# Performance work log

Hardware: AMD Instinct MI355X
Metric: run time of the kernel (lower is better)

## Reference

```python
import jax, jax.numpy as jnp
import numpy as np

B, S, HID = 1, 4096, 2048
NH, NKV, D = 16, 4, 128           # num_heads, num_kv_heads, head_dim
QPG = NH // NKV                   # q heads per kv group
GROUP = (QPG + 2) * D             # fused per-group width: Q..Q K V
TOTAL = NKV * GROUP


def setup_inputs() -> dict:
    key = jax.random.key(0)
    k0, k1, k2 = jax.random.split(key, 3)
    x = jax.random.normal(k0, (B, S, HID), dtype=jnp.float32)
    weight_qkv = jax.random.normal(k1, (TOTAL, HID), dtype=jnp.float32) * 0.02
    weight_proj = jax.random.normal(k2, (HID, NH * D), dtype=jnp.float32) * 0.02
    return {"x": x, "weight_qkv": weight_qkv, "weight_proj": weight_proj}


def reference(x, weight_qkv, weight_proj):
    b, s, _ = x.shape
    # fused QKV projection, grouped layout: [b, s, NKV, (QPG+2)*D]
    qkv = jnp.einsum('bsh,ph->bsp', x, weight_qkv).reshape(b, s, NKV, GROUP)
    q = qkv[..., : QPG * D].reshape(b, s, NKV, QPG, D)      # [b,s,g,q,d]
    k = qkv[..., QPG * D:(QPG + 1) * D]                      # [b,s,g,d]
    v = qkv[..., (QPG + 1) * D:]                             # [b,s,g,d]

    scale = 1.0 / jnp.sqrt(jnp.float32(D))
    # GQA causal attention (ring attention at cp_size=1 == full causal attn)
    scores = jnp.einsum('bsgqd,btgd->bgqst', q, k) * scale   # [b,g,q,s,s]
    causal = jnp.tril(jnp.ones((s, s), dtype=bool))
    scores = jnp.where(causal, scores, jnp.finfo(scores.dtype).min)
    attn = jax.nn.softmax(scores, axis=-1)
    out = jnp.einsum('bgqst,btgd->bsgqd', attn, v)           # [b,s,g,q,d]
    out = out.reshape(b, s, NH * D)
    return jnp.einsum('bse,he->bsh', out, weight_proj)       # [b,s,HID]
```

## Files before the change

### kernel.cpp

```cpp
#include <hip/hip_runtime.h>
#include <hip/hip_bf16.h>
#include <stdint.h>

typedef __attribute__((ext_vector_type(8))) short short8;
typedef __attribute__((ext_vector_type(4))) float f32x4;

#define S_LEN   4096
#define HID_DIM 2048
#define NHEAD   16
#define NKV     4
#define DHEAD   128
#define QPG     4
#define GROUP   768
#define TOTAL   3072

__device__ __forceinline__ ushort f2bf(float f) {
    union { float f; uint32_t u; } c; c.f = f;
    uint32_t u = c.u;
    u += 0x7fff + ((u >> 16) & 1);
    return (ushort)(u >> 16);
}

__device__ __forceinline__ void gld_lds16(const void* g, void* l) {
    __builtin_amdgcn_global_load_lds(
        (const __attribute__((address_space(1))) void*)g,
        (__attribute__((address_space(3))) void*)l, 16, 0, 0);
}

__global__ __launch_bounds__(256)
void cvt_f32_bf16(const float* __restrict__ src, ushort* __restrict__ dst,
                  int n4, int mode)
{
    int i = blockIdx.x * blockDim.x + threadIdx.x;
    int stride = gridDim.x * blockDim.x;
    for (; i < n4; i += stride) {
        float sc = 1.0f;
        if (mode == 1) {
            int row = i >> 9;
            sc = ((row % GROUP) < QPG * DHEAD) ? 0.088388347648318447f : 1.0f;
        }
        float4 v = ((const float4*)src)[i];
        ushort4 o;
        o.x = f2bf(v.x * sc); o.y = f2bf(v.y * sc);
        o.z = f2bf(v.z * sc); o.w = f2bf(v.w * sc);
        ((ushort4*)dst)[i] = o;
    }
}

__global__ __launch_bounds__(256)
void zero_f4(float4* __restrict__ p, int n4)
{
    int i = blockIdx.x * blockDim.x + threadIdx.x;
    int stride = gridDim.x * blockDim.x;
    float4 z = {0.f, 0.f, 0.f, 0.f};
    for (; i < n4; i += stride) p[i] = z;
}

__device__ __forceinline__ void store_c(ushort* C, size_t idx, float v) { C[idx] = f2bf(v); }
__device__ __forceinline__ void store_c(float*  C, size_t idx, float v) { C[idx] = v; }

template <typename OutT, bool WRITE_VT>
__global__ __launch_bounds__(256, 2)
void gemm_bt(const ushort* __restrict__ A, const ushort* __restrict__ B,
             OutT* __restrict__ C, ushort* __restrict__ VT,
             int M, int N, int K)
{
    __shared__ alignas(16) ushort Asl[128 * 32];
    __shared__ alignas(16) ushort Bsl[128 * 32];

    const int tid  = threadIdx.x;
    const int wave = tid >> 6;
    const int lane = tid & 63;
    const int quad = lane >> 4;
    const int l15  = lane & 15;
    const int wr   = wave >> 1;
    const int wc   = wave & 1;
    const int m0   = blockIdx.y * 128;
    const int n0   = blockIdx.x * 128;

    f32x4 acc[4][4];
#pragma unroll
    for (int i = 0; i < 4; i++)
#pragma unroll
        for (int j = 0; j < 4; j++) acc[i][j] = (f32x4)0.0f;

    for (int kb = 0; kb < K; kb += 32) {
        __syncthreads();
#pragma unroll
        for (int r = 0; r < 2; r++) {
            int idx = tid + r * 256;
            int row = idx >> 2, c8 = idx & 3;
            char* la = (char*)Asl + (size_t)(wave * 64 + r * 256) * 16;
            char* lb = (char*)Bsl + (size_t)(wave * 64 + r * 256) * 16;
            gld_lds16(A + (size_t)(m0 + row) * K + kb + c8 * 8, la);
            gld_lds16(B + (size_t)(n0 + row) * K + kb + c8 * 8, lb);
        }
        __syncthreads();

        short8 af[4], bf[4];
#pragma unroll
        for (int i = 0; i < 4; i++)
            af[i] = *(const short8*)(&Asl[(wr * 64 + i * 16 + l15) * 32 + quad * 8]);
#pragma unroll
        for (int j = 0; j < 4; j++)
            bf[j] = *(const short8*)(&Bsl[(wc * 64 + j * 16 + l15) * 32 + quad * 8]);
#pragma unroll
        for (int i = 0; i < 4; i++)
#pragma unroll
            for (int j = 0; j < 4; j++)
                acc[i][j] = __builtin_amdgcn_mfma_f32_16x16x32_bf16(
                    af[i], bf[j], acc[i][j], 0, 0, 0);
    }

#pragma unroll
    for (int i = 0; i < 4; i++)
#pragma unroll
        for (int j = 0; j < 4; j++)
#pragma unroll
            for (int r = 0; r < 4; r++) {
                int row = m0 + wr * 64 + i * 16 + quad * 4 + r;
                int col = n0 + wc * 64 + j * 16 + l15;
                store_c(C, (size_t)row * N + col, acc[i][j][r]);
            }

    if (WRITE_VT) {
        int cb = n0 >> 7;
        if (cb % 6 == 5) {
            int g = cb / 6;
#pragma unroll
            for (int i = 0; i < 4; i++)
#pragma unroll
                for (int j = 0; j < 4; j++) {
                    int d    = wc * 64 + j * 16 + l15;
                    int row0 = m0 + wr * 64 + i * 16 + quad * 4;
                    ushort4 pk;
                    pk.x = f2bf(acc[i][j][0]); pk.y = f2bf(acc[i][j][1]);
                    pk.z = f2bf(acc[i][j][2]); pk.w = f2bf(acc[i][j][3]);
                    *(ushort4*)(VT + (size_t)(g * 128 + d) * S_LEN + row0) = pk;
                }
        }
    }
}

__global__ __launch_bounds__(256, 2)
void flash_attn(const ushort* __restrict__ qkv, const ushort* __restrict__ VT,
                ushort* __restrict__ out, float* __restrict__ o_slot,
                float* __restrict__ l_slot)
{
    const int b    = blockIdx.x;
    const int head = b >> 5;
    const int pair = (b >> 1) & 15;
    const int half = b & 1;
    const int g    = head >> 2;
    const int qh   = head & 3;
    const int p_h  = 31 - pair;
    const int H    = 2 * p_h + 2;
    const int slot = head * 16 + pair;

    const int tid  = threadIdx.x;
    const int wave = tid >> 6;
    const int lane = tid & 63;
    const int quad = lane >> 4;
    const int l15  = lane & 15;

    __shared__ alignas(16) ushort Kl[64][136];
    __shared__ alignas(16) ushort Vt[128][72];
    __shared__ alignas(16) ushort Pl[4][32][72];

    int seg_p[2], seg_t0[2], seg_t1[2], seg_part[2];
    int nseg;
    if (half == 0) {
        nseg = 1;
        seg_p[0] = p_h;  seg_t0[0] = 0;  seg_t1[0] = 33;          seg_part[0] = 1;
    } else {
        nseg = 2;
        seg_p[0] = p_h;  seg_t0[0] = 33; seg_t1[0] = H;           seg_part[0] = 1;
        seg_p[1] = pair; seg_t0[1] = 0;  seg_t1[1] = 2 * pair + 2; seg_part[1] = 0;
    }

    const int koff = g * GROUP + QPG * DHEAD;

    for (int s = 0; s < nseg; s++) {
        const int p  = seg_p[s];
        const int t0 = seg_t0[s];
        const int t1 = seg_t1[s];
        const int q0 = p * 128;

        short8 qf[2][4];
#pragma unroll
        for (int mi = 0; mi < 2; mi++) {
            int row = q0 + wave * 32 + mi * 16 + l15;
            const ushort* qp = qkv + (size_t)row * TOTAL + g * GROUP + qh * DHEAD + quad * 8;
#pragma unroll
            for (int ks = 0; ks < 4; ks++)
                qf[mi][ks] = *(const short8*)(qp + ks * 32);
        }

        f32x4 o[2][8];
#pragma unroll
        for (int mi = 0; mi < 2; mi++)
#pragma unroll
            for (int df = 0; df < 8; df++) o[mi][df] = (f32x4)0.0f;
        float l_vec[2][4];
#pragma unroll
        for (int mi = 0; mi < 2; mi++)
#pragma unroll
            for (int r = 0; r < 4; r++) l_vec[mi][r] = 0.0f;

        float4 kpre[4], vpre[4];
#pragma unroll
        for (int r = 0; r < 4; r++) {
            int c = tid + r * 256;
            int kr = c >> 4, kc = c & 15;
            kpre[r] = *(const float4*)(qkv + (size_t)(t0 * 64 + kr) * TOTAL + koff + kc * 8);
            int vd = c >> 3, vc = c & 7;
            vpre[r] = *(const float4*)(VT + (size_t)(g * 128 + vd) * S_LEN + t0 * 64 + vc * 8);
        }

        for (int t = t0; t < t1; t++) {
            __syncthreads();
#pragma unroll
            for (int r = 0; r < 4; r++) {
                int c = tid + r * 256;
                int kr = c >> 4, kc = c & 15;
                *(float4*)(&Kl[kr][kc * 8]) = kpre[r];
                int vd = c >> 3, vc = c & 7;
                *(float4*)(&Vt[vd][vc * 8]) = vpre[r];
            }
            __syncthreads();

            if (t + 1 < t1) {
                const int j1 = (t + 1) * 64;
#pragma unroll
                for (int r = 0; r < 4; r++) {
                    int c = tid + r * 256;
                    int kr = c >> 4, kc = c & 15;
                    kpre[r] = *(const float4*)(qkv + (size_t)(j1 + kr) * TOTAL + koff + kc * 8);
                    int vd = c >> 3, vc = c & 7;
                    vpre[r] = *(const float4*)(VT + (size_t)(g * 128 + vd) * S_LEN + j1 + vc * 8);
                }
            }

            const int j0 = t * 64;
            f32x4 sacc[2][4];
#pragma unroll
            for (int mi = 0; mi < 2; mi++)
#pragma unroll
                for (int ni = 0; ni < 4; ni++) sacc[mi][ni] = (f32x4)0.0f;
#pragma unroll
            for (int ni = 0; ni < 4; ni++)
#pragma unroll
                for (int ks = 0; ks < 4; ks++) {
                    short8 kf = *(const short8*)(&Kl[ni * 16 + l15][ks * 32 + quad * 8]);
#pragma unroll
                    for (int mi = 0; mi < 2; mi++)
                        sacc[mi][ni] = __builtin_amdgcn_mfma_f32_16x16x32_bf16(
                            qf[mi][ks], kf, sacc[mi][ni], 0, 0, 0);
                }

#pragma unroll
            for (int mi = 0; mi < 2; mi++) {
                const int base = q0 + wave * 32 + mi * 16;
                if (j0 + 63 > base) {
#pragma unroll
                    for (int r = 0; r < 4; r++) {
                        int row_g = base + quad * 4 + r;
                        float rs = 0.0f;
#pragma unroll
                        for (int ni = 0; ni < 4; ni++) {
                            float e = __expf(sacc[mi][ni][r]);
                            int col_g = j0 + ni * 16 + l15;
                            e = (col_g > row_g) ? 0.0f : e;
                            sacc[mi][ni][r] = e;
                            rs += e;
                        }
                        l_vec[mi][r] += rs;
                    }
                } else {
#pragma unroll
                    for (int r = 0; r < 4; r++) {
                        float rs = 0.0f;
#pragma unroll
                        for (int ni = 0; ni < 4; ni++) {
                            float e = __expf(sacc[mi][ni][r]);
                            sacc[mi][ni][r] = e;
                            rs += e;
                        }
                        l_vec[mi][r] += rs;
                    }
                }
#pragma unroll
                for (int ni = 0; ni < 4; ni++)
#pragma unroll
                    for (int r = 0; r < 4; r++)
                        Pl[wave][mi * 16 + quad * 4 + r][ni * 16 + l15] =
                            f2bf(sacc[mi][ni][r]);
            }

#pragma unroll
            for (int ks = 0; ks < 2; ks++) {
                short8 pf[2];
#pragma unroll
                for (int mi = 0; mi < 2; mi++)
                    pf[mi] = *(const short8*)(&Pl[wave][mi * 16 + l15][ks * 32 + quad * 8]);
#pragma unroll
                for (int df = 0; df < 8; df++) {
                    short8 vf = *(const short8*)(&Vt[df * 16 + l15][ks * 32 + quad * 8]);
#pragma unroll
                    for (int mi = 0; mi < 2; mi++)
                        o[mi][df] = __builtin_amdgcn_mfma_f32_16x16x32_bf16(
                            pf[mi], vf, o[mi][df], 0, 0, 0);
                }
            }
        }

        if (seg_part[s]) {
#pragma unroll
            for (int mi = 0; mi < 2; mi++)
#pragma unroll
                for (int r = 0; r < 4; r++) {
                    int row_l = wave * 32 + mi * 16 + quad * 4 + r;
                    float l = l_vec[mi][r];
                    l += __shfl_xor(l, 1);
                    l += __shfl_xor(l, 2);
                    l += __shfl_xor(l, 4);
                    l += __shfl_xor(l, 8);
                    if (l15 == 0)
                        atomicAdd(&l_slot[slot * 128 + row_l], l);
#pragma unroll
                    for (int df = 0; df < 8; df++)
                        atomicAdd(&o_slot[((size_t)slot * 128 + row_l) * 128
                                          + df * 16 + l15], o[mi][df][r]);
                }
        } else {
#pragma unroll
            for (int mi = 0; mi < 2; mi++)
#pragma unroll
                for (int r = 0; r < 4; r++) {
                    float l = l_vec[mi][r];
                    l += __shfl_xor(l, 1);
                    l += __shfl_xor(l, 2);
                    l += __shfl_xor(l, 4);
                    l += __shfl_xor(l, 8);
                    float inv = 1.0f / l;
                    int row = q0 + wave * 32 + mi * 16 + quad * 4 + r;
#pragma unroll
                    for (int df = 0; df < 8; df++) {
                        float v = o[mi][df][r] * inv;
                        out[(size_t)row * (NHEAD * DHEAD) + head * DHEAD
                            + df * 16 + l15] = f2bf(v);
                    }
                }
        }
    }
}

__global__ __launch_bounds__(256)
void fixup_norm(const float* __restrict__ o_slot, const float* __restrict__ l_slot,
                ushort* __restrict__ attn)
{
    const int slot = blockIdx.x;
    const int head = slot >> 4;
    const int pair = slot & 15;
    const int q0   = (31 - pair) * 128;
    const int t    = threadIdx.x;
#pragma unroll 4
    for (int i = 0; i < 64; i++) {
        int idx = i * 256 + t;
        int row = idx >> 7, d = idx & 127;
        float l = l_slot[slot * 128 + row];
        float v = o_slot[(size_t)slot * 16384 + idx] / l;
        attn[(size_t)(q0 + row) * HID_DIM + head * DHEAD + d] = f2bf(v);
    }
}

extern "C" void kernel_launch(void* const* d_in, const int* in_sizes, int n_in,
                              void* d_out, int out_size, void* d_ws, size_t ws_size,
                              hipStream_t stream)
{
    const float* x     = (const float*)d_in[0];
    const float* wqkv  = (const float*)d_in[1];
    const float* wproj = (const float*)d_in[2];
    float* outp = (float*)d_out;

    const size_t n_x     = (size_t)S_LEN * HID_DIM;
    const size_t n_wqkv  = (size_t)TOTAL * HID_DIM;
    const size_t n_wproj = (size_t)HID_DIM * HID_DIM;
    const size_t n_qkv   = (size_t)S_LEN * TOTAL;
    const size_t n_attn  = (size_t)S_LEN * HID_DIM;

    ushort* xb     = (ushort*)d_ws;
    ushort* wqkvb  = xb + n_x;
    ushort* qkv    = wqkvb + n_wqkv;
    ushort* attn   = qkv + n_qkv;
    ushort* vt     = attn + n_attn;
    float* o_slot  = (float*)xb;
    float* l_slot  = (float*)wqkvb;
    ushort* wprojb = wqkvb;

    cvt_f32_bf16<<<2048, 256, 0, stream>>>(x, xb, (int)(n_x / 4), 0);
    cvt_f32_bf16<<<2048, 256, 0, stream>>>(wqkv, wqkvb, (int)(n_wqkv / 4), 1);

    gemm_bt<ushort, true><<<dim3(TOTAL / 128, S_LEN / 128), 256, 0, stream>>>(
        xb, wqkvb, qkv, vt, S_LEN, TOTAL, HID_DIM);

    zero_f4<<<1024, 256, 0, stream>>>((float4*)o_slot, 256 * 16384 / 4);
    zero_f4<<<64, 256, 0, stream>>>((float4*)l_slot, 256 * 128 / 4);

    flash_attn<<<512, 256, 0, stream>>>(qkv, vt, attn, o_slot, l_slot);
    fixup_norm<<<256, 256, 0, stream>>>(o_slot, l_slot, attn);

    cvt_f32_bf16<<<2048, 256, 0, stream>>>(wproj, wprojb, (int)(n_wproj / 4), 0);
    gemm_bt<float, false><<<dim3(HID_DIM / 128, S_LEN / 128), 256, 0, stream>>>(
        attn, wprojb, outp, nullptr, S_LEN, HID_DIM, HID_DIM);
}
```

Before: 428.0 us.

## Split causal attention work into thirds across 768 blocks with XCD-aware head mapping

Splits each paired causal attention workload (long+short query tiles, 66 KV tiles total) into three equal 22-tile chunks instead of two halves, launching 768 blocks at occupancy 3. Blocks are mapped so each XCD handles two heads, which improves K/V cache locality. More partial results now go through atomic accumulation slots (336 slots), and the partials are zeroed in one merged launch. The cost is more atomic traffic and a larger fixup pass, and the higher occupancy target may cause register spills.

```diff
diff --git a/kernel.cpp b/kernel.cpp
--- a/kernel.cpp
+++ b/kernel.cpp
@@ -13,6 +13,8 @@
 #define QPG     4
 #define GROUP   768
 #define TOTAL   3072
+
+#define NSLOT   336
 
 __device__ __forceinline__ ushort f2bf(float f) {
     union { float f; uint32_t u; } c; c.f = f;
@@ -142,20 +144,25 @@
     }
 }
 
-__global__ __launch_bounds__(256, 2)
+__global__ __launch_bounds__(256, 3)
 void flash_attn(const ushort* __restrict__ qkv, const ushort* __restrict__ VT,
                 ushort* __restrict__ out, float* __restrict__ o_slot,
                 float* __restrict__ l_slot)
 {
-    const int b    = blockIdx.x;
-    const int head = b >> 5;
-    const int pair = (b >> 1) & 15;
-    const int half = b & 1;
+    const int xcd  = blockIdx.x & 7;
+    const int ix   = blockIdx.x >> 3;
+    const int head = 2 * xcd + (ix >= 48 ? 1 : 0);
+    const int r48  = ix >= 48 ? ix - 48 : ix;
+    const int pair = r48 / 3;
+    const int third = r48 - pair * 3;
+
     const int g    = head >> 2;
     const int qh   = head & 3;
     const int p_h  = 31 - pair;
     const int H    = 2 * p_h + 2;
-    const int slot = head * 16 + pair;
+    const int L    = 2 * pair + 2;
+    const int c0   = third * 22;
+    const int c1   = c0 + 22;
 
     const int tid  = threadIdx.x;
     const int wave = tid >> 6;
@@ -165,17 +172,25 @@
 
     __shared__ alignas(16) ushort Kl[64][136];
     __shared__ alignas(16) ushort Vt[128][72];
-    __shared__ alignas(16) ushort Pl[4][32][72];
-
-    int seg_p[2], seg_t0[2], seg_t1[2], seg_part[2];
-    int nseg;
-    if (half == 0) {
-        nseg = 1;
-        seg_p[0] = p_h;  seg_t0[0] = 0;  seg_t1[0] = 33;          seg_part[0] = 1;
-    } else {
-        nseg = 2;
-        seg_p[0] = p_h;  seg_t0[0] = 33; seg_t1[0] = H;           seg_part[0] = 1;
-        seg_p[1] = pair; seg_t0[1] = 0;  seg_t1[1] = 2 * pair + 2; seg_part[1] = 0;
+    __shared__ alignas(16) ushort Pl[4][32][68];
+
+    int seg_p[2], seg_t0[2], seg_t1[2], seg_slot[2];
+    int nseg = 0;
+    {
+        int h1 = (c1 < H) ? c1 : H;
+        if (c0 < h1) {
+            seg_p[nseg] = p_h; seg_t0[nseg] = c0; seg_t1[nseg] = h1;
+            seg_slot[nseg] = head * 16 + pair;
+            nseg++;
+        }
+        int l0 = (c0 > H) ? c0 : H;
+        if (l0 < c1) {
+            int lt0 = l0 - H, lt1 = c1 - H;
+            int whole = (lt0 == 0) & (lt1 == L);
+            seg_p[nseg] = pair; seg_t0[nseg] = lt0; seg_t1[nseg] = lt1;
+            seg_slot[nseg] = whole ? -1 : (256 + head * 5 + (pair - 11));
+            nseg++;
+        }
     }
 
     const int koff = g * GROUP + QPG * DHEAD;
@@ -314,7 +329,8 @@
             }
         }
 
-        if (seg_part[s]) {
+        if (seg_slot[s] >= 0) {
+            const int sslot = seg_slot[s];
 #pragma unroll
             for (int mi = 0; mi < 2; mi++)
 #pragma unroll
@@ -326,10 +342,10 @@
                     l += __shfl_xor(l, 4);
                     l += __shfl_xor(l, 8);
                     if (l15 == 0)
-                        atomicAdd(&l_slot[slot * 128 + row_l], l);
+                        atomicAdd(&l_slot[sslot * 128 + row_l], l);
 #pragma unroll
                     for (int df = 0; df < 8; df++)
-                        atomicAdd(&o_slot[((size_t)slot * 128 + row_l) * 128
+                        atomicAdd(&o_slot[((size_t)sslot * 128 + row_l) * 128
                                           + df * 16 + l15], o[mi][df][r]);
                 }
         } else {
@@ -360,10 +376,16 @@
                 ushort* __restrict__ attn)
 {
     const int slot = blockIdx.x;
-    const int head = slot >> 4;
-    const int pair = slot & 15;
-    const int q0   = (31 - pair) * 128;
-    const int t    = threadIdx.x;
+    int head, q0;
+    if (slot < 256) {
+        head = slot >> 4;
+        q0   = (31 - (slot & 15)) * 128;
+    } else {
+        int s = slot - 256;
+        head = s / 5;
+        q0   = (11 + (s - head * 5)) * 128;
+    }
+    const int t = threadIdx.x;
 #pragma unroll 4
     for (int i = 0; i < 64; i++) {
         int idx = i * 256 + t;
@@ -394,8 +416,8 @@
     ushort* qkv    = wqkvb + n_wqkv;
     ushort* attn   = qkv + n_qkv;
     ushort* vt     = attn + n_attn;
-    float* o_slot  = (float*)xb;
-    float* l_slot  = (float*)wqkvb;
+    float* o_slot  = (float*)d_ws;
+    float* l_slot  = o_slot + (size_t)NSLOT * 16384;
     ushort* wprojb = wqkvb;
 
     cvt_f32_bf16<<<2048, 256, 0, stream>>>(x, xb, (int)(n_x / 4), 0);
@@ -404,11 +426,11 @@
     gemm_bt<ushort, true><<<dim3(TOTAL / 128, S_LEN / 128), 256, 0, stream>>>(
         xb, wqkvb, qkv, vt, S_LEN, TOTAL, HID_DIM);
 
-    zero_f4<<<1024, 256, 0, stream>>>((float4*)o_slot, 256 * 16384 / 4);
-    zero_f4<<<64, 256, 0, stream>>>((float4*)l_slot, 256 * 128 / 4);
-
-    flash_attn<<<512, 256, 0, stream>>>(qkv, vt, attn, o_slot, l_slot);
-    fixup_norm<<<256, 256, 0, stream>>>(o_slot, l_slot, attn);
+    zero_f4<<<2048, 256, 0, stream>>>((float4*)o_slot,
+                                      (int)(((size_t)NSLOT * 16384 + NSLOT * 128) / 4));
+
+    flash_attn<<<768, 256, 0, stream>>>(qkv, vt, attn, o_slot, l_slot);
+    fixup_norm<<<NSLOT, 256, 0, stream>>>(o_slot, l_slot, attn);
 
     cvt_f32_bf16<<<2048, 256, 0, stream>>>(wproj, wprojb, (int)(n_wproj / 4), 0);
     gemm_bt<float, false><<<dim3(HID_DIM / 128, S_LEN / 128), 256, 0, stream>>>(
```

Result: slower. 587.1 us (+37.2%).

## Double-buffer K/V LDS tiles with 32-key steps and MFMA priority hints

Applied to the files above, without the earlier changes.

Shrinks the flash-attention key tile from 64 to 32 and stores K/V into two LDS buffers, so the next tile is written while the current one is used. This cuts the two barriers per iteration down to one. It also raises wave priority around the MFMA blocks with s_setprio. The smaller tiles halve LDS use and register prefetch, which may raise occupancy, at the cost of twice as many loop iterations and more per-iteration overhead.

```diff
diff --git a/kernel.cpp b/kernel.cpp
--- a/kernel.cpp
+++ b/kernel.cpp
@@ -13,6 +13,8 @@
 #define QPG     4
 #define GROUP   768
 #define TOTAL   3072
+
+#define NSLOT   256
 
 __device__ __forceinline__ ushort f2bf(float f) {
     union { float f; uint32_t u; } c; c.f = f;
@@ -153,8 +155,8 @@
     const int half = b & 1;
     const int g    = head >> 2;
     const int qh   = head & 3;
-    const int p_h  = 31 - pair;
-    const int H    = 2 * p_h + 2;
+    const int H    = 128 - 4 * pair;
+    const int L    = 4 * pair + 4;
     const int slot = head * 16 + pair;
 
     const int tid  = threadIdx.x;
@@ -163,28 +165,27 @@
     const int quad = lane >> 4;
     const int l15  = lane & 15;
 
-    __shared__ alignas(16) ushort Kl[64][136];
-    __shared__ alignas(16) ushort Vt[128][72];
-    __shared__ alignas(16) ushort Pl[4][32][72];
+    __shared__ alignas(16) ushort Kl[2][32][136];
+    __shared__ alignas(16) ushort Vt[2][128][40];
+    __shared__ alignas(16) ushort Pl[4][32][36];
 
     int seg_p[2], seg_t0[2], seg_t1[2], seg_part[2];
     int nseg;
     if (half == 0) {
         nseg = 1;
-        seg_p[0] = p_h;  seg_t0[0] = 0;  seg_t1[0] = 33;          seg_part[0] = 1;
+        seg_p[0] = 31 - pair; seg_t0[0] = 0;  seg_t1[0] = 66; seg_part[0] = 1;
     } else {
         nseg = 2;
-        seg_p[0] = p_h;  seg_t0[0] = 33; seg_t1[0] = H;           seg_part[0] = 1;
-        seg_p[1] = pair; seg_t0[1] = 0;  seg_t1[1] = 2 * pair + 2; seg_part[1] = 0;
+        seg_p[0] = 31 - pair; seg_t0[0] = 66; seg_t1[0] = H;  seg_part[0] = 1;
+        seg_p[1] = pair;      seg_t0[1] = 0;  seg_t1[1] = L;  seg_part[1] = 0;
     }
 
     const int koff = g * GROUP + QPG * DHEAD;
 
     for (int s = 0; s < nseg; s++) {
-        const int p  = seg_p[s];
         const int t0 = seg_t0[s];
         const int t1 = seg_t1[s];
-        const int q0 = p * 128;
+        const int q0 = seg_p[s] * 128;
 
         short8 qf[2][4];
 #pragma unroll
@@ -207,67 +208,78 @@
 #pragma unroll
             for (int r = 0; r < 4; r++) l_vec[mi][r] = 0.0f;
 
-        float4 kpre[4], vpre[4];
-#pragma unroll
-        for (int r = 0; r < 4; r++) {
-            int c = tid + r * 256;
-            int kr = c >> 4, kc = c & 15;
-            kpre[r] = *(const float4*)(qkv + (size_t)(t0 * 64 + kr) * TOTAL + koff + kc * 8);
-            int vd = c >> 3, vc = c & 7;
-            vpre[r] = *(const float4*)(VT + (size_t)(g * 128 + vd) * S_LEN + t0 * 64 + vc * 8);
-        }
+        const int kr = tid >> 4, kc = tid & 15;
+        const int vd = tid >> 2, vc = tid & 3;
+
+        float4 kpre[2], vpre[2];
+#pragma unroll
+        for (int r = 0; r < 2; r++) {
+            kpre[r] = *(const float4*)(qkv + (size_t)(t0 * 32 + kr + r * 16) * TOTAL + koff + kc * 8);
+            vpre[r] = *(const float4*)(VT + (size_t)(g * 128 + vd + r * 64) * S_LEN + t0 * 32 + vc * 8);
+        }
+#pragma unroll
+        for (int r = 0; r < 2; r++) {
+            *(float4*)(&Kl[0][kr + r * 16][kc * 8]) = kpre[r];
+            *(float4*)(&Vt[0][vd + r * 64][vc * 8]) = vpre[r];
+        }
+        if (t0 + 1 < t1) {
+            const int j1 = (t0 + 1) * 32;
+#pragma unroll
+            for (int r = 0; r < 2; r++) {
+                kpre[r] = *(const float4*)(qkv + (size_t)(j1 + kr + r * 16) * TOTAL + koff + kc * 8);
+                vpre[r] = *(const float4*)(VT + (size_t)(g * 128 + vd + r * 64) * S_LEN + j1 + vc * 8);
+            }
+        }
+        __syncthreads();
 
         for (int t = t0; t < t1; t++) {
-            __syncthreads();
-#pragma unroll
-            for (int r = 0; r < 4; r++) {
-                int c = tid + r * 256;
-                int kr = c >> 4, kc = c & 15;
-                *(float4*)(&Kl[kr][kc * 8]) = kpre[r];
-                int vd = c >> 3, vc = c & 7;
-                *(float4*)(&Vt[vd][vc * 8]) = vpre[r];
+            const int cur = (t - t0) & 1;
+
+            if (t + 1 < t1) {
+#pragma unroll
+                for (int r = 0; r < 2; r++) {
+                    *(float4*)(&Kl[cur ^ 1][kr + r * 16][kc * 8]) = kpre[r];
+                    *(float4*)(&Vt[cur ^ 1][vd + r * 64][vc * 8]) = vpre[r];
+                }
+                if (t + 2 < t1) {
+                    const int j2 = (t + 2) * 32;
+#pragma unroll
+                    for (int r = 0; r < 2; r++) {
+                        kpre[r] = *(const float4*)(qkv + (size_t)(j2 + kr + r * 16) * TOTAL + koff + kc * 8);
+                        vpre[r] = *(const float4*)(VT + (size_t)(g * 128 + vd + r * 64) * S_LEN + j2 + vc * 8);
+                    }
+                }
             }
-            __syncthreads();
-
-            if (t + 1 < t1) {
-                const int j1 = (t + 1) * 64;
-#pragma unroll
-                for (int r = 0; r < 4; r++) {
-                    int c = tid + r * 256;
-                    int kr = c >> 4, kc = c & 15;
-                    kpre[r] = *(const float4*)(qkv + (size_t)(j1 + kr) * TOTAL + koff + kc * 8);
-                    int vd = c >> 3, vc = c & 7;
-                    vpre[r] = *(const float4*)(VT + (size_t)(g * 128 + vd) * S_LEN + j1 + vc * 8);
-                }
-            }
-
-            const int j0 = t * 64;
-            f32x4 sacc[2][4];
+
+            const int j0 = t * 32;
+            f32x4 sacc[2][2];
 #pragma unroll
             for (int mi = 0; mi < 2; mi++)
 #pragma unroll
-                for (int ni = 0; ni < 4; ni++) sacc[mi][ni] = (f32x4)0.0f;
-#pragma unroll
-            for (int ni = 0; ni < 4; ni++)
+                for (int ni = 0; ni < 2; ni++) sacc[mi][ni] = (f32x4)0.0f;
+            __builtin_amdgcn_s_setprio(1);
+#pragma unroll
+            for (int ni = 0; ni < 2; ni++)
 #pragma unroll
                 for (int ks = 0; ks < 4; ks++) {
-                    short8 kf = *(const short8*)(&Kl[ni * 16 + l15][ks * 32 + quad * 8]);
+                    short8 kf = *(const short8*)(&Kl[cur][ni * 16 + l15][ks * 32 + quad * 8]);
 #pragma unroll
                     for (int mi = 0; mi < 2; mi++)
                         sacc[mi][ni] = __builtin_amdgcn_mfma_f32_16x16x32_bf16(
                             qf[mi][ks], kf, sacc[mi][ni], 0, 0, 0);
                 }
+            __builtin_amdgcn_s_setprio(0);
 
 #pragma unroll
             for (int mi = 0; mi < 2; mi++) {
                 const int base = q0 + wave * 32 + mi * 16;
-                if (j0 + 63 > base) {
+                if (j0 + 31 > base) {
 #pragma unroll
                     for (int r = 0; r < 4; r++) {
                         int row_g = base + quad * 4 + r;
                         float rs = 0.0f;
 #pragma unroll
-                        for (int ni = 0; ni < 4; ni++) {
+                        for (int ni = 0; ni < 2; ni++) {
                             float e = __expf(sacc[mi][ni][r]);
                             int col_g = j0 + ni * 16 + l15;
                             e = (col_g > row_g) ? 0.0f : e;
@@ -281,7 +293,7 @@
                     for (int r = 0; r < 4; r++) {
                         float rs = 0.0f;
 #pragma unroll
-                        for (int ni = 0; ni < 4; ni++) {
+                        for (int ni = 0; ni < 2; ni++) {
                             float e = __expf(sacc[mi][ni][r]);
                             sacc[mi][ni][r] = e;
                             rs += e;
@@ -290,28 +302,29 @@
                     }
                 }
 #pragma unroll
-                for (int ni = 0; ni < 4; ni++)
+                for (int ni = 0; ni < 2; ni++)
 #pragma unroll
                     for (int r = 0; r < 4; r++)
                         Pl[wave][mi * 16 + quad * 4 + r][ni * 16 + l15] =
                             f2bf(sacc[mi][ni][r]);
             }
 
-#pragma unroll
-            for (int ks = 0; ks < 2; ks++) {
-                short8 pf[2];
+            short8 pf[2];
+#pragma unroll
+            for (int mi = 0; mi < 2; mi++)
+                pf[mi] = *(const short8*)(&Pl[wave][mi * 16 + l15][quad * 8]);
+            __builtin_amdgcn_s_setprio(1);
+#pragma unroll
+            for (int df = 0; df < 8; df++) {
+                short8 vf = *(const short8*)(&Vt[cur][df * 16 + l15][quad * 8]);
 #pragma unroll
                 for (int mi = 0; mi < 2; mi++)
-                    pf[mi] = *(const short8*)(&Pl[wave][mi * 16 + l15][ks * 32 + quad * 8]);
-#pragma unroll
-                for (int df = 0; df < 8; df++) {
-                    short8 vf = *(const short8*)(&Vt[df * 16 + l15][ks * 32 + quad * 8]);
-#pragma unroll
-                    for (int mi = 0; mi < 2; mi++)
-                        o[mi][df] = __builtin_amdgcn_mfma_f32_16x16x32_bf16(
-                            pf[mi], vf, o[mi][df], 0, 0, 0);
-                }
+                    o[mi][df] = __builtin_amdgcn_mfma_f32_16x16x32_bf16(
+                        pf[mi], vf, o[mi][df], 0, 0, 0);
             }
+            __builtin_amdgcn_s_setprio(0);
+
+            __syncthreads();
         }
 
         if (seg_part[s]) {
@@ -361,8 +374,7 @@
 {
     const int slot = blockIdx.x;
     const int head = slot >> 4;
-    const int pair = slot & 15;
-    const int q0   = (31 - pair) * 128;
+    const int q0   = (31 - (slot & 15)) * 128;
     const int t    = threadIdx.x;
 #pragma unroll 4
     for (int i = 0; i < 64; i++) {
@@ -408,7 +420,7 @@
     zero_f4<<<64, 256, 0, stream>>>((float4*)l_slot, 256 * 128 / 4);
 
     flash_attn<<<512, 256, 0, stream>>>(qkv, vt, attn, o_slot, l_slot);
-    fixup_norm<<<256, 256, 0, stream>>>(o_slot, l_slot, attn);
+    fixup_norm<<<NSLOT, 256, 0, stream>>>(o_slot, l_slot, attn);
 
     cvt_f32_bf16<<<2048, 256, 0, stream>>>(wproj, wprojb, (int)(n_wproj / 4), 0);
     gemm_bt<float, false><<<dim3(HID_DIM / 128, S_LEN / 128), 256, 0, stream>>>(
```

Result: faster. 409.7 us (-4.3%).
